# Kernel tuning notes

Measured on AMD Instinct MI355X. Metric: run time of the kernel, lower is better.

## Reference

```python
import jax, jax.numpy as jnp
import numpy as np

N_ITER = 5
NMF_EPS = 1e-20
IP_EPS = 1e-20

M, J, I, K = 2, 2000, 2049, 8  # channels == sources, frames, freq bins, NMF bases


def setup_inputs() -> dict:
    key = jax.random.key(0)
    k1, k2, k3 = jax.random.split(key, 3)
    X = jax.random.normal(k1, (M, J, I, 2), dtype=jnp.float32)
    lo = 1e-08
    T0 = jax.random.uniform(k2, (I, K, M), dtype=jnp.float32) * (1 - lo) + lo
    V0 = jax.random.uniform(k3, (K, J, M), dtype=jnp.float32) * (1 - lo) + lo
    return {"X": X, "T0": T0, "V0": V0}


def nmf_update(T, V, Y, eps):
    # T: (I,K), V: (K,J), Y: (I,J) complex
    P = jnp.abs(Y) ** 2                       # power spectrogram (I,J)
    R = T @ V                                  # low-rank model (I,J)
    T = T * jnp.sqrt(((P / (R * R)) @ V.T) / ((1.0 / R) @ V.T))
    T = jnp.maximum(T, eps)
    R = T @ V
    V = V * jnp.sqrt((T.T @ (P / (R * R))) / (T.T @ (1.0 / R)))
    V = jnp.maximum(V, eps)
    R = T @ V
    return T, V, R


def reference(X, T0, V0):
    Mc, Jc, Ic, _ = X.shape
    N = Mc
    # view_as_complex(X.permute(2,0,1,3)) -> (I, M, J) complex
    Xc = jnp.transpose(X[..., 0] + 1j * X[..., 1], (2, 0, 1)).astype(jnp.complex64)
    eye_M = jnp.eye(Mc, dtype=jnp.complex64)
    W = jnp.broadcast_to(eye_M, (Ic, N, Mc))   # (I, N, M)
    T, V = T0, V0

    def body(carry, _):
        W, T, V = carry
        Y = jnp.einsum('inm,imj->inj', W, Xc)  # (I, N, J)
        for n in range(N):
            Tn, Vn, Rn = nmf_update(T[:, :, n], V[:, :, n], Y[:, n, :], NMF_EPS)
            T = T.at[:, :, n].set(Tn)
            V = V.at[:, :, n].set(Vn)
            inv_Rn = 1.0 / (Rn + IP_EPS)                       # (I, J)
            Xw = Xc * jnp.sqrt(inv_Rn)[:, None, :]             # (I, M, J)
            D = jnp.einsum('imj,ikj->imk', Xw, jnp.conj(Xw)) / Jc  # (I, M, M)
            Dreg = D + IP_EPS * eye_M
            A = jnp.einsum('inm,imk->ink', W, Dreg)            # (I, M, M)
            e_n = jnp.broadcast_to(eye_M[:, n], (Ic, Mc))
            b = jnp.linalg.solve(A, e_n[..., None])[..., 0]    # (I, M)
            quad = jnp.einsum('im,imk,ik->i', jnp.conj(b), Dreg, b)
            denom = jnp.sqrt(jnp.real(quad) + IP_EPS)          # (I,)
            W = W.at[:, n, :].set(jnp.conj(b / denom[:, None]))
        return (W, T, V), None

    (W, T, V), _ = jax.lax.scan(body, (W, T, V), None, length=N_ITER)
    Y = jnp.einsum('inm,imj->inj', W, Xc)                      # (I, N, J)
    Yp = jnp.transpose(Y, (1, 2, 0))                           # (N, J, I)
    return jnp.stack([jnp.real(Yp), jnp.imag(Yp)], axis=-1)    # (N, J, I, 2)
```

## Files before the change

kernel.cpp:

```cpp
#include <hip/hip_runtime.h>
#include <hip/hip_fp16.h>

#define M_CH 2
#define J_F 2000
#define I_F 2049
#define K_B 8
#define N_IT 5
#define NMF_EPS 1e-20f
#define IP_EPS 1e-20f

#define NB_TILE (65 * 63)
#define NB_INIT 128

__device__ __forceinline__ float2 h2f(unsigned u) {
  __half2 h = *reinterpret_cast<__half2*>(&u);
  return __half22float2(h);
}
__device__ __forceinline__ float4 h4f(unsigned lo, unsigned hi) {
  float2 a = h2f(lo), b = h2f(hi);
  return make_float4(a.x, a.y, b.x, b.y);
}
__device__ __forceinline__ unsigned f2h(float a, float b) {
  __half2 h = __floats2half2_rn(a, b);
  return *reinterpret_cast<unsigned*>(&h);
}

template<int PK>
__global__ __launch_bounds__(256) void k_setup(const float2* __restrict__ X,
                                               const float* __restrict__ T0,
                                               const float* __restrict__ V0,
                                               float* __restrict__ T,
                                               float* __restrict__ V,
                                               float* __restrict__ W,
                                               __half* __restrict__ Xht,
                                               __half* __restrict__ Xhj) {
  int b = blockIdx.x;
  const int tid = threadIdx.x;
  if (b < NB_TILE) {
    if (!PK) return;
    __shared__ float4 Tl[32][33];
    const int i0 = (b % 65) * 32, j0 = (b / 65) * 32;
    const int la = tid & 31, su = tid >> 5;
#pragma unroll
    for (int p = 0; p < 4; ++p) {
      int jj = su + p * 8;
      int i = i0 + la, j = j0 + jj;
      if (i < I_F && j < J_F) {
        float2 a = X[(size_t)j * I_F + i];
        float2 c = X[(size_t)(J_F + j) * I_F + i];
        float4 x = make_float4(a.x, a.y, c.x, c.y);
        Tl[la][jj] = x;
        *(uint2*)(Xhj + ((size_t)j * I_F + i) * 4) =
            make_uint2(f2h(x.x, x.y), f2h(x.z, x.w));
      }
    }
    __syncthreads();
#pragma unroll
    for (int p = 0; p < 4; ++p) {
      int ii = su + p * 8;
      int i = i0 + ii, j = j0 + la;
      if (i < I_F && j < J_F) {
        float4 x = Tl[ii][la];
        *(uint2*)(Xht + ((size_t)i * J_F + j) * 4) =
            make_uint2(f2h(x.x, x.y), f2h(x.z, x.w));
      }
    }
    return;
  }
  b -= NB_TILE;
  int t = b * 256 + tid;
  const int stride = NB_INIT * 256;
  for (int idx = t; idx < 2 * I_F * K_B; idx += stride) {
    int n = idx / (I_F * K_B);
    int r = idx % (I_F * K_B);
    int i = r / K_B, k = r % K_B;
    T[idx] = T0[(i * K_B + k) * M_CH + n];
  }
  for (int idx = t; idx < 2 * K_B * J_F; idx += stride) {
    int n = idx / (K_B * J_F);
    int r = idx % (K_B * J_F);
    int k = r / J_F, j = r % J_F;
    V[idx] = V0[(k * J_F + j) * M_CH + n];
  }
  for (int i = t; i < I_F; i += stride) {
    W[i * 8 + 0] = 1.f; W[i * 8 + 1] = 0.f; W[i * 8 + 2] = 0.f; W[i * 8 + 3] = 0.f;
    W[i * 8 + 4] = 0.f; W[i * 8 + 5] = 0.f; W[i * 8 + 6] = 1.f; W[i * 8 + 7] = 0.f;
  }
}

template<int PK>
__device__ __forceinline__ void t_phase(const int i, const __half* __restrict__ Xht,
                                        const float2* __restrict__ X,
                                        const float4 w0, const float4 w1,
                                        float* __restrict__ T, const float* __restrict__ V,
                                        float (*red)[32]) {
  const int tid = threadIdx.x;
  float tr0[K_B], tr1[K_B];
#pragma unroll
  for (int k = 0; k < K_B; ++k) {
    tr0[k] = T[(size_t)i * 8 + k];
    tr1[k] = T[((size_t)I_F + i) * 8 + k];
  }
  float num0[K_B] = {}, den0[K_B] = {}, num1[K_B] = {}, den1[K_B] = {};
  if (PK) {
    const __half* xrow = Xht + (size_t)i * J_F * 4;
    for (int j2 = tid; j2 < J_F / 2; j2 += 256) {
      const int j = j2 * 2;
      uint4 raw = *(const uint4*)(xrow + (size_t)j * 4);
      float4 xa = h4f(raw.x, raw.y);
      float4 xb = h4f(raw.z, raw.w);
      float2 v0p[K_B], v1p[K_B];
      float R0a = 0.f, R0b = 0.f, R1a = 0.f, R1b = 0.f;
#pragma unroll
      for (int k = 0; k < K_B; ++k) {
        v0p[k] = *(const float2*)&V[(size_t)k * J_F + j];
        v1p[k] = *(const float2*)&V[(size_t)(K_B + k) * J_F + j];
        R0a += tr0[k] * v0p[k].x; R0b += tr0[k] * v0p[k].y;
        R1a += tr1[k] * v1p[k].x; R1b += tr1[k] * v1p[k].y;
      }
      float yr, yi;
      yr = w0.x * xa.x - w0.y * xa.y + w0.z * xa.z - w0.w * xa.w;
      yi = w0.x * xa.y + w0.y * xa.x + w0.z * xa.w + w0.w * xa.z;
      float p0a = yr * yr + yi * yi;
      yr = w1.x * xa.x - w1.y * xa.y + w1.z * xa.z - w1.w * xa.w;
      yi = w1.x * xa.y + w1.y * xa.x + w1.z * xa.w + w1.w * xa.z;
      float p1a = yr * yr + yi * yi;
      yr = w0.x * xb.x - w0.y * xb.y + w0.z * xb.z - w0.w * xb.w;
      yi = w0.x * xb.y + w0.y * xb.x + w0.z * xb.w + w0.w * xb.z;
      float p0b = yr * yr + yi * yi;
      yr = w1.x * xb.x - w1.y * xb.y + w1.z * xb.z - w1.w * xb.w;
      yi = w1.x * xb.y + w1.y * xb.x + w1.z * xb.w + w1.w * xb.z;
      float p1b = yr * yr + yi * yi;
      float a0a = p0a / (R0a * R0a), b0a = 1.f / R0a;
      float a1a = p1a / (R1a * R1a), b1a = 1.f / R1a;
      float a0b = p0b / (R0b * R0b), b0b = 1.f / R0b;
      float a1b = p1b / (R1b * R1b), b1b = 1.f / R1b;
#pragma unroll
      for (int k = 0; k < K_B; ++k) {
        num0[k] += a0a * v0p[k].x + a0b * v0p[k].y;
        den0[k] += b0a * v0p[k].x + b0b * v0p[k].y;
        num1[k] += a1a * v1p[k].x + a1b * v1p[k].y;
        den1[k] += b1a * v1p[k].x + b1b * v1p[k].y;
      }
    }
  } else {
    for (int j = tid; j < J_F; j += 256) {
      float2 a = X[(size_t)j * I_F + i];
      float2 c = X[(size_t)(J_F + j) * I_F + i];
      float4 x = make_float4(a.x, a.y, c.x, c.y);
      float yr = w0.x * x.x - w0.y * x.y + w0.z * x.z - w0.w * x.w;
      float yi = w0.x * x.y + w0.y * x.x + w0.z * x.w + w0.w * x.z;
      float p0 = yr * yr + yi * yi;
      float zr = w1.x * x.x - w1.y * x.y + w1.z * x.z - w1.w * x.w;
      float zi = w1.x * x.y + w1.y * x.x + w1.z * x.w + w1.w * x.z;
      float p1 = zr * zr + zi * zi;
      float v0[K_B], v1[K_B];
      float R0 = 0.f, R1 = 0.f;
#pragma unroll
      for (int k = 0; k < K_B; ++k) {
        v0[k] = V[(size_t)k * J_F + j];         R0 += tr0[k] * v0[k];
        v1[k] = V[(size_t)(K_B + k) * J_F + j]; R1 += tr1[k] * v1[k];
      }
      float a0 = p0 / (R0 * R0), b0 = 1.0f / R0;
      float a1 = p1 / (R1 * R1), b1 = 1.0f / R1;
#pragma unroll
      for (int k = 0; k < K_B; ++k) {
        num0[k] += a0 * v0[k]; den0[k] += b0 * v0[k];
        num1[k] += a1 * v1[k]; den1[k] += b1 * v1[k];
      }
    }
  }
  const int lane = tid & 63, wid = tid >> 6;
#pragma unroll
  for (int k = 0; k < K_B; ++k) {
    float a0 = num0[k], b0 = den0[k], a1 = num1[k], b1 = den1[k];
#pragma unroll
    for (int off = 32; off > 0; off >>= 1) {
      a0 += __shfl_xor(a0, off, 64);
      b0 += __shfl_xor(b0, off, 64);
      a1 += __shfl_xor(a1, off, 64);
      b1 += __shfl_xor(b1, off, 64);
    }
    if (lane == 0) {
      red[wid][k] = a0; red[wid][8 + k] = b0;
      red[wid][16 + k] = a1; red[wid][24 + k] = b1;
    }
  }
  __syncthreads();
  if (tid < 32) red[0][tid] = red[0][tid] + red[1][tid] + red[2][tid] + red[3][tid];
  __syncthreads();
  if (tid < 16) {
    int n = tid >> 3, k = tid & 7;
    float nu = red[0][n * 16 + k];
    float de = red[0][n * 16 + 8 + k];
    size_t idx = ((size_t)n * I_F + i) * 8 + k;
    float told = T[idx];
    T[idx] = fmaxf(told * sqrtf(nu / de), NMF_EPS);
  }
}

template<int PK>
__device__ __forceinline__ void d_phase(const int i, const __half* __restrict__ Xht,
                                        const float2* __restrict__ X,
                                        const float* __restrict__ T,
                                        const float* __restrict__ V,
                                        float* __restrict__ W,
                                        float (*red)[32], float* wrow) {
  const int tid = threadIdx.x;
  float tr0[K_B], tr1[K_B];
#pragma unroll
  for (int k = 0; k < K_B; ++k) {
    tr0[k] = T[(size_t)i * K_B + k];
    tr1[k] = T[((size_t)I_F + i) * K_B + k];
  }
  float acc[8] = {};
  if (PK) {
    const __half* xrow = Xht + (size_t)i * J_F * 4;
    for (int j2 = tid; j2 < J_F / 2; j2 += 256) {
      const int j = j2 * 2;
      uint4 raw = *(const uint4*)(xrow + (size_t)j * 4);
      float4 xa = h4f(raw.x, raw.y);
      float4 xb = h4f(raw.z, raw.w);
      float R0a = 0.f, R0b = 0.f, R1a = 0.f, R1b = 0.f;
#pragma unroll
      for (int k = 0; k < K_B; ++k) {
        float2 v0p = *(const float2*)&V[(size_t)k * J_F + j];
        float2 v1p = *(const float2*)&V[(size_t)(K_B + k) * J_F + j];
        R0a += tr0[k] * v0p.x; R0b += tr0[k] * v0p.y;
        R1a += tr1[k] * v1p.x; R1b += tr1[k] * v1p.y;
      }
      float wv0a = 1.0f / (R0a + IP_EPS), wv0b = 1.0f / (R0b + IP_EPS);
      float wv1a = 1.0f / (R1a + IP_EPS), wv1b = 1.0f / (R1b + IP_EPS);
      float p00a = xa.x * xa.x + xa.y * xa.y, p00b = xb.x * xb.x + xb.y * xb.y;
      float p11a = xa.z * xa.z + xa.w * xa.w, p11b = xb.z * xb.z + xb.w * xb.w;
      float pra = xa.x * xa.z + xa.y * xa.w, prb = xb.x * xb.z + xb.y * xb.w;
      float pia = xa.y * xa.z - xa.x * xa.w, pib = xb.y * xb.z - xb.x * xb.w;
      acc[0] += wv0a * p00a + wv0b * p00b;
      acc[1] += wv0a * p11a + wv0b * p11b;
      acc[2] += wv0a * pra + wv0b * prb;
      acc[3] += wv0a * pia + wv0b * pib;
      acc[4] += wv1a * p00a + wv1b * p00b;
      acc[5] += wv1a * p11a + wv1b * p11b;
      acc[6] += wv1a * pra + wv1b * prb;
      acc[7] += wv1a * pia + wv1b * pib;
    }
  } else {
    for (int j = tid; j < J_F; j += 256) {
      float2 a = X[(size_t)j * I_F + i];
      float2 c = X[(size_t)(J_F + j) * I_F + i];
      float4 x = make_float4(a.x, a.y, c.x, c.y);
      float R0 = 0.f, R1 = 0.f;
#pragma unroll
      for (int k = 0; k < K_B; ++k) {
        R0 += tr0[k] * V[(size_t)k * J_F + j];
        R1 += tr1[k] * V[(size_t)(K_B + k) * J_F + j];
      }
      float wv0 = 1.0f / (R0 + IP_EPS);
      float wv1 = 1.0f / (R1 + IP_EPS);
      float p00 = x.x * x.x + x.y * x.y;
      float p11 = x.z * x.z + x.w * x.w;
      float pr = x.x * x.z + x.y * x.w;
      float pi = x.y * x.z - x.x * x.w;
      acc[0] += wv0 * p00; acc[1] += wv0 * p11; acc[2] += wv0 * pr; acc[3] += wv0 * pi;
      acc[4] += wv1 * p00; acc[5] += wv1 * p11; acc[6] += wv1 * pr; acc[7] += wv1 * pi;
    }
  }
  const int lane = tid & 63, wid = tid >> 6;
#pragma unroll
  for (int v = 0; v < 8; ++v) {
    float a = acc[v];
#pragma unroll
    for (int off = 32; off > 0; off >>= 1) a += __shfl_xor(a, off, 64);
    if (lane == 0) red[wid][v] = a;
  }
  __syncthreads();
  if (tid < 8) red[0][tid] = red[0][tid] + red[1][tid] + red[2][tid] + red[3][tid];
  __syncthreads();
  if (tid == 0) {
    float4 wa = ((const float4*)W)[i * 2];
    float4 wb = ((const float4*)W)[i * 2 + 1];
    float w00r = wa.x, w00i = wa.y, w01r = wa.z, w01i = wa.w;
    float w10r = wb.x, w10i = wb.y, w11r = wb.z, w11i = wb.w;
    const float invJ = 1.0f / (float)J_F;
#pragma unroll
    for (int n = 0; n < 2; ++n) {
      float d00 = red[0][n * 4 + 0] * invJ + IP_EPS;
      float d11 = red[0][n * 4 + 1] * invJ + IP_EPS;
      float d01r = red[0][n * 4 + 2] * invJ;
      float d01i = red[0][n * 4 + 3] * invJ;
      float A00r = w00r * d00 + (w01r * d01r + w01i * d01i);
      float A00i = w00i * d00 + (w01i * d01r - w01r * d01i);
      float A01r = (w00r * d01r - w00i * d01i) + w01r * d11;
      float A01i = (w00r * d01i + w00i * d01r) + w01i * d11;
      float A10r = w10r * d00 + (w11r * d01r + w11i * d01i);
      float A10i = w10i * d00 + (w11i * d01r - w11r * d01i);
      float A11r = (w10r * d01r - w10i * d01i) + w11r * d11;
      float A11i = (w10r * d01i + w10i * d01r) + w11i * d11;
      float detr = (A00r * A11r - A00i * A11i) - (A01r * A10r - A01i * A10i);
      float deti = (A00r * A11i + A00i * A11r) - (A01r * A10i + A01i * A10r);
      float idet = 1.0f / (detr * detr + deti * deti);
      float n0r, n0i, n1r, n1i;
      if (n == 0) { n0r = A11r; n0i = A11i; n1r = -A10r; n1i = -A10i; }
      else        { n0r = -A01r; n0i = -A01i; n1r = A00r; n1i = A00i; }
      float b0r = (n0r * detr + n0i * deti) * idet;
      float b0i = (n0i * detr - n0r * deti) * idet;
      float b1r = (n1r * detr + n1i * deti) * idet;
      float b1i = (n1i * detr - n1r * deti) * idet;
      float cr = d01r * b1r - d01i * b1i;
      float ci = d01r * b1i + d01i * b1r;
      float quad = d00 * (b0r * b0r + b0i * b0i) + d11 * (b1r * b1r + b1i * b1i)
                 + 2.0f * (b0r * cr + b0i * ci);
      float s = 1.0f / sqrtf(quad + IP_EPS);
      if (n == 0) { w00r = b0r * s; w00i = -b0i * s; w01r = b1r * s; w01i = -b1i * s; }
      else        { w10r = b0r * s; w10i = -b0i * s; w11r = b1r * s; w11i = -b1i * s; }
    }
    ((float4*)W)[i * 2]     = make_float4(w00r, w00i, w01r, w01i);
    ((float4*)W)[i * 2 + 1] = make_float4(w10r, w10i, w11r, w11i);
    wrow[0] = w00r; wrow[1] = w00i; wrow[2] = w01r; wrow[3] = w01i;
    wrow[4] = w10r; wrow[5] = w10i; wrow[6] = w11r; wrow[7] = w11i;
  }
  __syncthreads();
}

template<int PK>
__global__ __launch_bounds__(256) void k_T(const __half* __restrict__ Xht,
                                           const float2* __restrict__ X,
                                           const float* __restrict__ W,
                                           float* __restrict__ T,
                                           const float* __restrict__ V) {
  __shared__ float red[4][32];
  const int i = blockIdx.x;
  const float4 w0 = ((const float4*)W)[i * 2];
  const float4 w1 = ((const float4*)W)[i * 2 + 1];
  t_phase<PK>(i, Xht, X, w0, w1, T, V, red);
}

template<int PK>
__global__ __launch_bounds__(256) void k_D(const __half* __restrict__ Xht,
                                           const float2* __restrict__ X,
                                           const float* __restrict__ T,
                                           const float* __restrict__ V,
                                           float* __restrict__ W) {
  __shared__ float red[4][32];
  __shared__ float wrow[8];
  d_phase<PK>(blockIdx.x, Xht, X, T, V, W, red, wrow);
}

template<int PK>
__global__ __launch_bounds__(256) void k_DT(const __half* __restrict__ Xht,
                                            const float2* __restrict__ X,
                                            float* __restrict__ T,
                                            const float* __restrict__ V,
                                            float* __restrict__ W) {
  __shared__ float red[4][32];
  __shared__ float wrow[8];
  const int i = blockIdx.x;
  d_phase<PK>(i, Xht, X, T, V, W, red, wrow);
  const float4 w0 = make_float4(wrow[0], wrow[1], wrow[2], wrow[3]);
  const float4 w1 = make_float4(wrow[4], wrow[5], wrow[6], wrow[7]);
  __syncthreads();
  t_phase<PK>(i, Xht, X, w0, w1, T, V, red);
}

template<int PK>
__global__ __launch_bounds__(256) void k_V(const __half* __restrict__ Xhj,
                                           const float2* __restrict__ X,
                                           const float* __restrict__ W,
                                           const float* __restrict__ T,
                                           float* __restrict__ V) {
  const int j = blockIdx.x;
  const int tid = threadIdx.x;
  float vold0[K_B], vold1[K_B];
#pragma unroll
  for (int k = 0; k < K_B; ++k) {
    vold0[k] = V[(size_t)k * J_F + j];
    vold1[k] = V[(size_t)(K_B + k) * J_F + j];
  }
  float num0[K_B] = {}, den0[K_B] = {}, num1[K_B] = {}, den1[K_B] = {};
  const float* T1 = T + (size_t)I_F * K_B;
  const __half* xcol = Xhj + (size_t)j * I_F * 4;
  for (int i = tid; i < I_F; i += 256) {
    float4 x;
    if (PK) {
      uint2 raw = *(const uint2*)(xcol + (size_t)i * 4);
      x = h4f(raw.x, raw.y);
    } else {
      float2 a = X[(size_t)j * I_F + i];
      float2 c = X[(size_t)(J_F + j) * I_F + i];
      x = make_float4(a.x, a.y, c.x, c.y);
    }
    const float4 wa = ((const float4*)W)[i * 2];
    const float4 wb = ((const float4*)W)[i * 2 + 1];
    float yr = wa.x * x.x - wa.y * x.y + wa.z * x.z - wa.w * x.w;
    float yi = wa.x * x.y + wa.y * x.x + wa.z * x.w + wa.w * x.z;
    float p0 = yr * yr + yi * yi;
    float zr = wb.x * x.x - wb.y * x.y + wb.z * x.z - wb.w * x.w;
    float zi = wb.x * x.y + wb.y * x.x + wb.z * x.w + wb.w * x.z;
    float p1 = zr * zr + zi * zi;
    const float4 ta = *(const float4*)&T[i * 8];
    const float4 tb = *(const float4*)&T[i * 8 + 4];
    const float4 tc = *(const float4*)&T1[i * 8];
    const float4 td = *(const float4*)&T1[i * 8 + 4];
    float t0[K_B] = {ta.x, ta.y, ta.z, ta.w, tb.x, tb.y, tb.z, tb.w};
    float t1[K_B] = {tc.x, tc.y, tc.z, tc.w, td.x, td.y, td.z, td.w};
    float R0 = 0.f, R1 = 0.f;
#pragma unroll
    for (int k = 0; k < K_B; ++k) { R0 += t0[k] * vold0[k]; R1 += t1[k] * vold1[k]; }
    float a0 = p0 / (R0 * R0), b0 = 1.0f / R0;
    float a1 = p1 / (R1 * R1), b1 = 1.0f / R1;
#pragma unroll
    for (int k = 0; k < K_B; ++k) {
      num0[k] += a0 * t0[k]; den0[k] += b0 * t0[k];
      num1[k] += a1 * t1[k]; den1[k] += b1 * t1[k];
    }
  }
  __shared__ float red[4][32];
  const int lane = tid & 63, wid = tid >> 6;
#pragma unroll
  for (int k = 0; k < K_B; ++k) {
    float a0 = num0[k], b0 = den0[k], a1 = num1[k], b1 = den1[k];
#pragma unroll
    for (int off = 32; off > 0; off >>= 1) {
      a0 += __shfl_xor(a0, off, 64);
      b0 += __shfl_xor(b0, off, 64);
      a1 += __shfl_xor(a1, off, 64);
      b1 += __shfl_xor(b1, off, 64);
    }
    if (lane == 0) {
      red[wid][k] = a0; red[wid][8 + k] = b0;
      red[wid][16 + k] = a1; red[wid][24 + k] = b1;
    }
  }
  __syncthreads();
  if (tid < 32) red[0][tid] = red[0][tid] + red[1][tid] + red[2][tid] + red[3][tid];
  __syncthreads();
  if (tid < 16) {
    int n = tid >> 3, k = tid & 7;
    float nu = red[0][n * 16 + k];
    float de = red[0][n * 16 + 8 + k];
    size_t idx = ((size_t)n * K_B + k) * J_F + j;
    float vo = V[idx];
    V[idx] = fmaxf(vo * sqrtf(nu / de), NMF_EPS);
  }
}

template<int PK>
__global__ __launch_bounds__(256) void k_final(const __half* __restrict__ Xhj,
                                               const float2* __restrict__ X,
                                               const float* __restrict__ W,
                                               float2* __restrict__ out) {
  const int i = blockIdx.x * 256 + threadIdx.x;
  if (i >= I_F) return;
  const float4 wa = ((const float4*)W)[i * 2];
  const float4 wb = ((const float4*)W)[i * 2 + 1];
  const int j0 = blockIdx.y * 8;
  const int jend = min(8, J_F - j0);
  for (int jj = 0; jj < jend; ++jj) {
    const int j = j0 + jj;
    float4 x;
    if (PK) {
      uint2 raw = *(const uint2*)(Xhj + ((size_t)j * I_F + i) * 4);
      x = h4f(raw.x, raw.y);
    } else {
      float2 a = X[(size_t)j * I_F + i];
      float2 c = X[(size_t)(J_F + j) * I_F + i];
      x = make_float4(a.x, a.y, c.x, c.y);
    }
    float y0r = wa.x * x.x - wa.y * x.y + wa.z * x.z - wa.w * x.w;
    float y0i = wa.x * x.y + wa.y * x.x + wa.z * x.w + wa.w * x.z;
    out[(size_t)j * I_F + i] = make_float2(y0r, y0i);
    float y1r = wb.x * x.x - wb.y * x.y + wb.z * x.z - wb.w * x.w;
    float y1i = wb.x * x.y + wb.y * x.x + wb.z * x.w + wb.w * x.z;
    out[(size_t)(J_F + j) * I_F + i] = make_float2(y1r, y1i);
  }
}

extern "C" void kernel_launch(void* const* d_in, const int* in_sizes, int n_in,
                              void* d_out, int out_size, void* d_ws, size_t ws_size,
                              hipStream_t stream) {
  const float2* X = (const float2*)d_in[0];
  const float* T0 = (const float*)d_in[1];
  const float* V0 = (const float*)d_in[2];
  float2* outp = (float2*)d_out;
  char* ws = (char*)d_ws;
  size_t off = 0;
  auto alloc = [&](size_t bytes) -> void* {
    void* p = ws + off;
    off = (off + bytes + 255) & ~(size_t)255;
    return p;
  };
  float* W = (float*)alloc((size_t)I_F * 8 * 4);
  float* T = (float*)alloc((size_t)2 * I_F * K_B * 4);
  float* V = (float*)alloc((size_t)2 * K_B * J_F * 4);
  const size_t xh_sz = (size_t)J_F * I_F * 8;
  __half* Xht = nullptr;
  __half* Xhj = nullptr;
  if (off + 2 * xh_sz + 512 <= ws_size) {
    Xht = (__half*)alloc(xh_sz);
    Xhj = (__half*)alloc(xh_sz);
  }
  const int NBS = NB_TILE + NB_INIT;

  if (Xht) {
    k_setup<1><<<NBS, 256, 0, stream>>>(X, T0, V0, T, V, W, Xht, Xhj);
    k_T<1><<<I_F, 256, 0, stream>>>(Xht, X, W, T, V);
    for (int it = 0; it < N_IT; ++it) {
      k_V<1><<<J_F, 256, 0, stream>>>(Xhj, X, W, T, V);
      if (it < N_IT - 1)
        k_DT<1><<<I_F, 256, 0, stream>>>(Xht, X, T, V, W);
      else
        k_D<1><<<I_F, 256, 0, stream>>>(Xht, X, T, V, W);
    }
    k_final<1><<<dim3(9, 250), 256, 0, stream>>>(Xhj, X, W, outp);
  } else {
    k_setup<0><<<NBS, 256, 0, stream>>>(X, T0, V0, T, V, W, nullptr, nullptr);
    k_T<0><<<I_F, 256, 0, stream>>>(nullptr, X, W, T, V);
    for (int it = 0; it < N_IT; ++it) {
      k_V<0><<<J_F, 256, 0, stream>>>(nullptr, X, W, T, V);
      if (it < N_IT - 1)
        k_DT<0><<<I_F, 256, 0, stream>>>(nullptr, X, T, V, W);
      else
        k_D<0><<<I_F, 256, 0, stream>>>(nullptr, X, T, V, W);
    }
    k_final<0><<<dim3(9, 250), 256, 0, stream>>>(nullptr, X, W, outp);
  }
}
```

Before: 467.0 us.

## Keep a half-precision V copy, transpose T to k-major, widen D-phase loop

Adds a half-precision mirror of V, written at setup and after each V update. The T and D phases read it instead of the fp32 V, halving the bytes fetched per V access. T is stored k-major so the column-parallel V kernel reads T with coalesced per-k loads. The D phase now processes four frames per thread with wider loads. The price is extra writes for Vh, reduced precision in the R reconstruction inside the T and D phases, and an added block barrier at the end of t_phase.

```diff
diff --git a/kernel.cpp b/kernel.cpp
--- a/kernel.cpp
+++ b/kernel.cpp
@@ -31,6 +31,7 @@
                                                const float* __restrict__ V0,
                                                float* __restrict__ T,
                                                float* __restrict__ V,
+                                               __half* __restrict__ Vh,
                                                float* __restrict__ W,
                                                __half* __restrict__ Xht,
                                                __half* __restrict__ Xhj) {
@@ -70,17 +71,19 @@
   b -= NB_TILE;
   int t = b * 256 + tid;
   const int stride = NB_INIT * 256;
-  for (int idx = t; idx < 2 * I_F * K_B; idx += stride) {
-    int n = idx / (I_F * K_B);
-    int r = idx % (I_F * K_B);
-    int i = r / K_B, k = r % K_B;
+  for (int idx = t; idx < 2 * K_B * I_F; idx += stride) {
+    int n = idx / (K_B * I_F);
+    int r = idx % (K_B * I_F);
+    int k = r / I_F, i = r % I_F;
     T[idx] = T0[(i * K_B + k) * M_CH + n];
   }
   for (int idx = t; idx < 2 * K_B * J_F; idx += stride) {
     int n = idx / (K_B * J_F);
     int r = idx % (K_B * J_F);
     int k = r / J_F, j = r % J_F;
-    V[idx] = V0[(k * J_F + j) * M_CH + n];
+    float v = V0[(k * J_F + j) * M_CH + n];
+    V[idx] = v;
+    Vh[idx] = __float2half(v);
   }
   for (int i = t; i < I_F; i += stride) {
     W[i * 8 + 0] = 1.f; W[i * 8 + 1] = 0.f; W[i * 8 + 2] = 0.f; W[i * 8 + 3] = 0.f;
@@ -92,29 +95,30 @@
 __device__ __forceinline__ void t_phase(const int i, const __half* __restrict__ Xht,
                                         const float2* __restrict__ X,
                                         const float4 w0, const float4 w1,
-                                        float* __restrict__ T, const float* __restrict__ V,
+                                        float* __restrict__ T,
+                                        const float* __restrict__ V,
+                                        const __half* __restrict__ Vh,
                                         float (*red)[32]) {
   const int tid = threadIdx.x;
   float tr0[K_B], tr1[K_B];
 #pragma unroll
   for (int k = 0; k < K_B; ++k) {
-    tr0[k] = T[(size_t)i * 8 + k];
-    tr1[k] = T[((size_t)I_F + i) * 8 + k];
+    tr0[k] = T[(size_t)k * I_F + i];
+    tr1[k] = T[(size_t)(K_B + k) * I_F + i];
   }
   float num0[K_B] = {}, den0[K_B] = {}, num1[K_B] = {}, den1[K_B] = {};
   if (PK) {
-    const __half* xrow = Xht + (size_t)i * J_F * 4;
     for (int j2 = tid; j2 < J_F / 2; j2 += 256) {
       const int j = j2 * 2;
-      uint4 raw = *(const uint4*)(xrow + (size_t)j * 4);
+      uint4 raw = *(const uint4*)(Xht + ((size_t)i * J_F + j) * 4);
       float4 xa = h4f(raw.x, raw.y);
       float4 xb = h4f(raw.z, raw.w);
       float2 v0p[K_B], v1p[K_B];
       float R0a = 0.f, R0b = 0.f, R1a = 0.f, R1b = 0.f;
 #pragma unroll
       for (int k = 0; k < K_B; ++k) {
-        v0p[k] = *(const float2*)&V[(size_t)k * J_F + j];
-        v1p[k] = *(const float2*)&V[(size_t)(K_B + k) * J_F + j];
+        v0p[k] = h2f(*(const unsigned*)(Vh + (size_t)k * J_F + j));
+        v1p[k] = h2f(*(const unsigned*)(Vh + (size_t)(K_B + k) * J_F + j));
         R0a += tr0[k] * v0p[k].x; R0b += tr0[k] * v0p[k].y;
         R1a += tr1[k] * v1p[k].x; R1b += tr1[k] * v1p[k].y;
       }
@@ -193,10 +197,11 @@
     int n = tid >> 3, k = tid & 7;
     float nu = red[0][n * 16 + k];
     float de = red[0][n * 16 + 8 + k];
-    size_t idx = ((size_t)n * I_F + i) * 8 + k;
+    size_t idx = ((size_t)(n * K_B + k)) * I_F + i;
     float told = T[idx];
     T[idx] = fmaxf(told * sqrtf(nu / de), NMF_EPS);
   }
+  __syncthreads();
 }
 
 template<int PK>
@@ -204,45 +209,59 @@
                                         const float2* __restrict__ X,
                                         const float* __restrict__ T,
                                         const float* __restrict__ V,
+                                        const __half* __restrict__ Vh,
                                         float* __restrict__ W,
                                         float (*red)[32], float* wrow) {
   const int tid = threadIdx.x;
   float tr0[K_B], tr1[K_B];
 #pragma unroll
   for (int k = 0; k < K_B; ++k) {
-    tr0[k] = T[(size_t)i * K_B + k];
-    tr1[k] = T[((size_t)I_F + i) * K_B + k];
+    tr0[k] = T[(size_t)k * I_F + i];
+    tr1[k] = T[(size_t)(K_B + k) * I_F + i];
   }
   float acc[8] = {};
   if (PK) {
-    const __half* xrow = Xht + (size_t)i * J_F * 4;
-    for (int j2 = tid; j2 < J_F / 2; j2 += 256) {
-      const int j = j2 * 2;
-      uint4 raw = *(const uint4*)(xrow + (size_t)j * 4);
-      float4 xa = h4f(raw.x, raw.y);
-      float4 xb = h4f(raw.z, raw.w);
-      float R0a = 0.f, R0b = 0.f, R1a = 0.f, R1b = 0.f;
+    for (int q = tid; q < J_F / 4; q += 256) {
+      const int j = q * 4;
+      uint4 ra = *(const uint4*)(Xht + ((size_t)i * J_F + j) * 4);
+      uint4 rb = *(const uint4*)(Xht + ((size_t)i * J_F + j + 2) * 4);
+      float4 xa = h4f(ra.x, ra.y);
+      float4 xb = h4f(ra.z, ra.w);
+      float4 xc = h4f(rb.x, rb.y);
+      float4 xd = h4f(rb.z, rb.w);
+      float R0a = 0.f, R0b = 0.f, R0c = 0.f, R0d = 0.f;
+      float R1a = 0.f, R1b = 0.f, R1c = 0.f, R1d = 0.f;
 #pragma unroll
       for (int k = 0; k < K_B; ++k) {
-        float2 v0p = *(const float2*)&V[(size_t)k * J_F + j];
-        float2 v1p = *(const float2*)&V[(size_t)(K_B + k) * J_F + j];
-        R0a += tr0[k] * v0p.x; R0b += tr0[k] * v0p.y;
-        R1a += tr1[k] * v1p.x; R1b += tr1[k] * v1p.y;
+        uint2 u0 = *(const uint2*)(Vh + (size_t)k * J_F + j);
+        uint2 u1 = *(const uint2*)(Vh + (size_t)(K_B + k) * J_F + j);
+        float2 pa = h2f(u0.x), pb = h2f(u0.y);
+        float2 qa = h2f(u1.x), qb = h2f(u1.y);
+        R0a += tr0[k] * pa.x; R0b += tr0[k] * pa.y;
+        R0c += tr0[k] * pb.x; R0d += tr0[k] * pb.y;
+        R1a += tr1[k] * qa.x; R1b += tr1[k] * qa.y;
+        R1c += tr1[k] * qb.x; R1d += tr1[k] * qb.y;
       }
       float wv0a = 1.0f / (R0a + IP_EPS), wv0b = 1.0f / (R0b + IP_EPS);
+      float wv0c = 1.0f / (R0c + IP_EPS), wv0d = 1.0f / (R0d + IP_EPS);
       float wv1a = 1.0f / (R1a + IP_EPS), wv1b = 1.0f / (R1b + IP_EPS);
+      float wv1c = 1.0f / (R1c + IP_EPS), wv1d = 1.0f / (R1d + IP_EPS);
       float p00a = xa.x * xa.x + xa.y * xa.y, p00b = xb.x * xb.x + xb.y * xb.y;
+      float p00c = xc.x * xc.x + xc.y * xc.y, p00d = xd.x * xd.x + xd.y * xd.y;
       float p11a = xa.z * xa.z + xa.w * xa.w, p11b = xb.z * xb.z + xb.w * xb.w;
+      float p11c = xc.z * xc.z + xc.w * xc.w, p11d = xd.z * xd.z + xd.w * xd.w;
       float pra = xa.x * xa.z + xa.y * xa.w, prb = xb.x * xb.z + xb.y * xb.w;
+      float prc = xc.x * xc.z + xc.y * xc.w, prd = xd.x * xd.z + xd.y * xd.w;
       float pia = xa.y * xa.z - xa.x * xa.w, pib = xb.y * xb.z - xb.x * xb.w;
-      acc[0] += wv0a * p00a + wv0b * p00b;
-      acc[1] += wv0a * p11a + wv0b * p11b;
-      acc[2] += wv0a * pra + wv0b * prb;
-      acc[3] += wv0a * pia + wv0b * pib;
-      acc[4] += wv1a * p00a + wv1b * p00b;
-      acc[5] += wv1a * p11a + wv1b * p11b;
-      acc[6] += wv1a * pra + wv1b * prb;
-      acc[7] += wv1a * pia + wv1b * pib;
+      float pic = xc.y * xc.z - xc.x * xc.w, pid = xd.y * xd.z - xd.x * xd.w;
+      acc[0] += (wv0a * p00a + wv0b * p00b) + (wv0c * p00c + wv0d * p00d);
+      acc[1] += (wv0a * p11a + wv0b * p11b) + (wv0c * p11c + wv0d * p11d);
+      acc[2] += (wv0a * pra + wv0b * prb) + (wv0c * prc + wv0d * prd);
+      acc[3] += (wv0a * pia + wv0b * pib) + (wv0c * pic + wv0d * pid);
+      acc[4] += (wv1a * p00a + wv1b * p00b) + (wv1c * p00c + wv1d * p00d);
+      acc[5] += (wv1a * p11a + wv1b * p11b) + (wv1c * p11c + wv1d * p11d);
+      acc[6] += (wv1a * pra + wv1b * prb) + (wv1c * prc + wv1d * prd);
+      acc[7] += (wv1a * pia + wv1b * pib) + (wv1c * pic + wv1d * pid);
     }
   } else {
     for (int j = tid; j < J_F; j += 256) {
@@ -327,12 +346,13 @@
                                            const float2* __restrict__ X,
                                            const float* __restrict__ W,
                                            float* __restrict__ T,
-                                           const float* __restrict__ V) {
+                                           const float* __restrict__ V,
+                                           const __half* __restrict__ Vh) {
   __shared__ float red[4][32];
   const int i = blockIdx.x;
   const float4 w0 = ((const float4*)W)[i * 2];
   const float4 w1 = ((const float4*)W)[i * 2 + 1];
-  t_phase<PK>(i, Xht, X, w0, w1, T, V, red);
+  t_phase<PK>(i, Xht, X, w0, w1, T, V, Vh, red);
 }
 
 template<int PK>
@@ -340,10 +360,11 @@
                                            const float2* __restrict__ X,
                                            const float* __restrict__ T,
                                            const float* __restrict__ V,
+                                           const __half* __restrict__ Vh,
                                            float* __restrict__ W) {
   __shared__ float red[4][32];
   __shared__ float wrow[8];
-  d_phase<PK>(blockIdx.x, Xht, X, T, V, W, red, wrow);
+  d_phase<PK>(blockIdx.x, Xht, X, T, V, Vh, W, red, wrow);
 }
 
 template<int PK>
@@ -351,15 +372,16 @@
                                             const float2* __restrict__ X,
                                             float* __restrict__ T,
                                             const float* __restrict__ V,
+                                            const __half* __restrict__ Vh,
                                             float* __restrict__ W) {
   __shared__ float red[4][32];
   __shared__ float wrow[8];
   const int i = blockIdx.x;
-  d_phase<PK>(i, Xht, X, T, V, W, red, wrow);
+  d_phase<PK>(i, Xht, X, T, V, Vh, W, red, wrow);
   const float4 w0 = make_float4(wrow[0], wrow[1], wrow[2], wrow[3]);
   const float4 w1 = make_float4(wrow[4], wrow[5], wrow[6], wrow[7]);
   __syncthreads();
-  t_phase<PK>(i, Xht, X, w0, w1, T, V, red);
+  t_phase<PK>(i, Xht, X, w0, w1, T, V, Vh, red);
 }
 
 template<int PK>
@@ -367,7 +389,8 @@
                                            const float2* __restrict__ X,
                                            const float* __restrict__ W,
                                            const float* __restrict__ T,
-                                           float* __restrict__ V) {
+                                           float* __restrict__ V,
+                                           __half* __restrict__ Vh) {
   const int j = blockIdx.x;
   const int tid = threadIdx.x;
   float vold0[K_B], vold1[K_B];
@@ -377,7 +400,6 @@
     vold1[k] = V[(size_t)(K_B + k) * J_F + j];
   }
   float num0[K_B] = {}, den0[K_B] = {}, num1[K_B] = {}, den1[K_B] = {};
-  const float* T1 = T + (size_t)I_F * K_B;
   const __half* xcol = Xhj + (size_t)j * I_F * 4;
   for (int i = tid; i < I_F; i += 256) {
     float4 x;
@@ -397,15 +419,15 @@
     float zr = wb.x * x.x - wb.y * x.y + wb.z * x.z - wb.w * x.w;
     float zi = wb.x * x.y + wb.y * x.x + wb.z * x.w + wb.w * x.z;
     float p1 = zr * zr + zi * zi;
-    const float4 ta = *(const float4*)&T[i * 8];
-    const float4 tb = *(const float4*)&T[i * 8 + 4];
-    const float4 tc = *(const float4*)&T1[i * 8];
-    const float4 td = *(const float4*)&T1[i * 8 + 4];
-    float t0[K_B] = {ta.x, ta.y, ta.z, ta.w, tb.x, tb.y, tb.z, tb.w};
-    float t1[K_B] = {tc.x, tc.y, tc.z, tc.w, td.x, td.y, td.z, td.w};
+    float t0[K_B], t1[K_B];
     float R0 = 0.f, R1 = 0.f;
 #pragma unroll
-    for (int k = 0; k < K_B; ++k) { R0 += t0[k] * vold0[k]; R1 += t1[k] * vold1[k]; }
+    for (int k = 0; k < K_B; ++k) {
+      t0[k] = T[(size_t)k * I_F + i];
+      t1[k] = T[(size_t)(K_B + k) * I_F + i];
+      R0 += t0[k] * vold0[k];
+      R1 += t1[k] * vold1[k];
+    }
     float a0 = p0 / (R0 * R0), b0 = 1.0f / R0;
     float a1 = p1 / (R1 * R1), b1 = 1.0f / R1;
 #pragma unroll
@@ -438,9 +460,11 @@
     int n = tid >> 3, k = tid & 7;
     float nu = red[0][n * 16 + k];
     float de = red[0][n * 16 + 8 + k];
-    size_t idx = ((size_t)n * K_B + k) * J_F + j;
+    size_t idx = ((size_t)(n * K_B + k)) * J_F + j;
     float vo = V[idx];
-    V[idx] = fmaxf(vo * sqrtf(nu / de), NMF_EPS);
+    float vn = fmaxf(vo * sqrtf(nu / de), NMF_EPS);
+    V[idx] = vn;
+    Vh[idx] = __float2half(vn);
   }
 }
 
@@ -490,8 +514,9 @@
     return p;
   };
   float* W = (float*)alloc((size_t)I_F * 8 * 4);
-  float* T = (float*)alloc((size_t)2 * I_F * K_B * 4);
+  float* T = (float*)alloc((size_t)2 * K_B * I_F * 4);
   float* V = (float*)alloc((size_t)2 * K_B * J_F * 4);
+  __half* Vh = (__half*)alloc((size_t)2 * K_B * J_F * 2);
   const size_t xh_sz = (size_t)J_F * I_F * 8;
   __half* Xht = nullptr;
   __half* Xhj = nullptr;
@@ -502,25 +527,25 @@
   const int NBS = NB_TILE + NB_INIT;
 
   if (Xht) {
-    k_setup<1><<<NBS, 256, 0, stream>>>(X, T0, V0, T, V, W, Xht, Xhj);
-    k_T<1><<<I_F, 256, 0, stream>>>(Xht, X, W, T, V);
+    k_setup<1><<<NBS, 256, 0, stream>>>(X, T0, V0, T, V, Vh, W, Xht, Xhj);
+    k_T<1><<<I_F, 256, 0, stream>>>(Xht, X, W, T, V, Vh);
     for (int it = 0; it < N_IT; ++it) {
-      k_V<1><<<J_F, 256, 0, stream>>>(Xhj, X, W, T, V);
+      k_V<1><<<J_F, 256, 0, stream>>>(Xhj, X, W, T, V, Vh);
       if (it < N_IT - 1)
-        k_DT<1><<<I_F, 256, 0, stream>>>(Xht, X, T, V, W);
+        k_DT<1><<<I_F, 256, 0, stream>>>(Xht, X, T, V, Vh, W);
       else
-        k_D<1><<<I_F, 256, 0, stream>>>(Xht, X, T, V, W);
+        k_D<1><<<I_F, 256, 0, stream>>>(Xht, X, T, V, Vh, W);
     }
     k_final<1><<<dim3(9, 250), 256, 0, stream>>>(Xhj, X, W, outp);
   } else {
-    k_setup<0><<<NBS, 256, 0, stream>>>(X, T0, V0, T, V, W, nullptr, nullptr);
-    k_T<0><<<I_F, 256, 0, stream>>>(nullptr, X, W, T, V);
+    k_setup<0><<<NBS, 256, 0, stream>>>(X, T0, V0, T, V, Vh, W, nullptr, nullptr);
+    k_T<0><<<I_F, 256, 0, stream>>>(nullptr, X, W, T, V, Vh);
     for (int it = 0; it < N_IT; ++it) {
-      k_V<0><<<J_F, 256, 0, stream>>>(nullptr, X, W, T, V);
+      k_V<0><<<J_F, 256, 0, stream>>>(nullptr, X, W, T, V, Vh);
       if (it < N_IT - 1)
-        k_DT<0><<<I_F, 256, 0, stream>>>(nullptr, X, T, V, W);
+        k_DT<0><<<I_F, 256, 0, stream>>>(nullptr, X, T, V, Vh, W);
       else
-        k_D<0><<<I_F, 256, 0, stream>>>(nullptr, X, T, V, W);
+        k_D<0><<<I_F, 256, 0, stream>>>(nullptr, X, T, V, Vh, W);
     }
     k_final<0><<<dim3(9, 250), 256, 0, stream>>>(nullptr, X, W, outp);
   }
```

Result: faster. 422.7 us (median of 3 runs) (-9.5%).
